# Kernel tuning notes

Measured on AMD Instinct MI355X. Metric: run time of the kernel, lower is better.

Reference implementation:

```python
import jax, jax.numpy as jnp
import numpy as np

SORB = 64      # spin orbitals (sequence length)
NELE = 32      # electrons
H = 512        # num_hiddens
B = 4096       # batch
ALPHA = NELE // 2                      # = beta = 16 (spin-up / spin-down electrons)
MIN_I = min(SORB - 2 * ALPHA, 2 * ALPHA)  # = 32; symmetry mask active for i >= MIN_I
EPS = 1e-12


def setup_inputs() -> dict:
    key = jax.random.key(0)
    ks = jax.random.split(key, 10)
    s_in = 1.0 / np.sqrt(2.0)
    s_h = 1.0 / np.sqrt(H)
    return {
        "x": jax.random.randint(ks[0], (B, SORB), 0, 2, dtype=jnp.int32),  # occupancies {0,1}
        "W_ih0": jax.random.normal(ks[1], (3 * H, 2), jnp.float32) * s_in,   # GRU layer0 input weights (r,z,n)
        "W_hh0": jax.random.normal(ks[2], (3 * H, H), jnp.float32) * s_h,
        "W_ih1": jax.random.normal(ks[3], (3 * H, H), jnp.float32) * s_h,    # GRU layer1
        "W_hh1": jax.random.normal(ks[4], (3 * H, H), jnp.float32) * s_h,
        "W_amp": jax.random.normal(ks[5], (2, H), jnp.float32) * s_h,
        "b_amp": jax.random.normal(ks[6], (2,), jnp.float32) * 0.01,
        "W_phase": jax.random.normal(ks[7], (2, H), jnp.float32) * s_h,
        "b_phase": jax.random.normal(ks[8], (2,), jnp.float32) * 0.01,
    }


def _gru_cell(x_in, h, Wih, Whh):
    # PyTorch GRU (bias=False), gate order r, z, n
    gi = x_in @ Wih.T          # (B, 3H)
    gh = h @ Whh.T             # (B, 3H)
    r = jax.nn.sigmoid(gi[:, :H] + gh[:, :H])
    z = jax.nn.sigmoid(gi[:, H:2 * H] + gh[:, H:2 * H])
    n = jnp.tanh(gi[:, 2 * H:] + r * gh[:, 2 * H:])
    return (1.0 - z) * n + z * h


def reference(x, W_ih0, W_hh0, W_ih1, W_hh1, W_amp, b_amp, W_phase, b_phase):
    dt = W_ih0.dtype
    bits = x.astype(jnp.int32)           # (B, SORB) occupancies
    nb = bits.shape[0]

    def step(carry, inp):
        h0, h1, x0, amp, phase, nup, ndn = carry
        i, b_i = inp                      # site index, occupancy bits (B,)
        h0n = _gru_cell(x0, h0, W_ih0, W_hh0)
        h1n = _gru_cell(h0n, h1, W_ih1, W_hh1)
        y = h1n                           # (B, H)
        # amplitude: sqrt(softmax(linear))
        y_amp = jnp.sqrt(jax.nn.softmax(y @ W_amp.T + b_amp, axis=1))   # (B, 2)
        # phase: pi * softsign(linear)
        ph = y @ W_phase.T + b_phase
        y_ph = jnp.pi * ph / (1.0 + jnp.abs(ph))
        # particle-number symmetry mask (alpha == beta spin sectors)
        is_even = (i % 2) == 0            # even sites: spin-up, odd: spin-down
        cnt = jnp.where(is_even, nup, ndn)
        lower = (ALPHA - SORB // 2 + i // 2).astype(dt)
        occ_ok = (cnt < ALPHA).astype(dt)
        unocc_ok = (cnt > lower).astype(dt)
        mask = jnp.stack([unocc_ok, occ_ok], axis=1)
        masked = y_amp * mask
        masked = masked / jnp.sqrt(jnp.sum(masked * masked, axis=1, keepdims=True) + EPS)
        y_amp = jnp.where(i >= MIN_I, masked, y_amp)
        # accumulate conditional amplitude / phase at the sampled occupancy
        sel_a = jnp.take_along_axis(y_amp, b_i[:, None], axis=1)[:, 0]
        sel_p = jnp.take_along_axis(y_ph, b_i[:, None], axis=1)[:, 0]
        amp = amp * sel_a
        phase = phase + sel_p
        bf = b_i.astype(dt)
        nup = nup + jnp.where(is_even, bf, 0.0)
        ndn = ndn + jnp.where(is_even, 0.0, bf)
        x0n = jax.nn.one_hot(b_i, 2, dtype=dt)  # next-step GRU input
        return (h0n, h1n, x0n, amp, phase, nup, ndn), None

    init = (
        jnp.zeros((nb, H), dt), jnp.zeros((nb, H), dt), jnp.zeros((nb, 2), dt),
        jnp.ones((nb,), dt), jnp.zeros((nb,), dt), jnp.zeros((nb,), dt), jnp.zeros((nb,), dt),
    )
    xs = (jnp.arange(SORB), bits.T)       # scan over sites
    (_, _, _, amp, phase, _, _), _ = jax.lax.scan(step, init, xs)
    # complex wavefunction psi = amp * exp(1j*phase); returned as real pair (amp, phase)
    return jnp.stack([amp, phase], axis=-1)
```

## Files before the change

kernel.cpp:

```cpp
#include <hip/hip_runtime.h>
#include <hip/hip_bf16.h>

#define SORB  64
#define HID   512
#define BATCH 4096
#define N3H   1536
#define KD    512
#define BK    64
#define PI_F  3.14159265358979f

typedef _Float16 half8 __attribute__((ext_vector_type(8)));
typedef float    floatx4 __attribute__((ext_vector_type(4)));

__device__ __forceinline__ void gload16(const void* g, void* l) {
    __builtin_amdgcn_global_load_lds(
        (const __attribute__((address_space(1))) void*)g,
        (__attribute__((address_space(3))) void*)l, 16, 0, 0);
}
#define SCHED_FENCE() __builtin_amdgcn_sched_barrier(0)

__device__ __forceinline__ float sigmoidf_(float x) { return 1.f / (1.f + __expf(-x)); }
__device__ __forceinline__ float tanhf_(float x) {
    x = fminf(fmaxf(x, -15.f), 15.f);
    const float e2 = __expf(2.f * x);
    return (e2 - 1.f) / (e2 + 1.f);
}

__global__ __launch_bounds__(256) void convw_kernel(
    const float* __restrict__ w0, const float* __restrict__ w1, const float* __restrict__ w2,
    _Float16* __restrict__ o0, _Float16* __restrict__ o1, _Float16* __restrict__ o2)
{
    const int i = blockIdx.x * 256 + threadIdx.x;
    if (i < N3H * KD) {
        o0[i] = (_Float16)w0[i];
        o1[i] = (_Float16)w1[i];
        o2[i] = (_Float16)w2[i];
    }
}

__global__ __launch_bounds__(256) void init_kernel(
    float* __restrict__ amp, float* __restrict__ phase,
    int* __restrict__ nup, int* __restrict__ ndn)
{
    const int i = blockIdx.x * 256 + threadIdx.x;
    if (i < BATCH) { amp[i] = 1.f; phase[i] = 0.f; nup[i] = 0; ndn[i] = 0; }
}

__global__ __launch_bounds__(256) void step1_kernel(
    const _Float16* __restrict__ h0h_c, const _Float16* __restrict__ wh0,
    const float* __restrict__ Wih0, const int* __restrict__ bits,
    _Float16* __restrict__ h0h_n, int step)
{
    const int j0 = blockIdx.x * 64;
    const int m0 = blockIdx.y * 64;

    __shared__ __align__(16) _Float16 Bs[2][192 * BK];

    const int tid  = threadIdx.x;
    const int lane = tid & 63;
    const int wid  = tid >> 6;
    const int wm   = wid >> 1, wj = wid & 1;
    const int ku   = lane >> 4;

    floatx4 acc[2][2][3];
    const floatx4 z4 = {0.f, 0.f, 0.f, 0.f};
#pragma unroll
    for (int a = 0; a < 2; ++a)
#pragma unroll
        for (int b = 0; b < 2; ++b)
#pragma unroll
            for (int g = 0; g < 3; ++g) acc[a][b][g] = z4;

    const _Float16* b_srcp[6];
#pragma unroll
    for (int k2 = 0; k2 < 6; ++k2) {
        const int p = tid + k2 * 256, row = p >> 3, c = (p & 7) ^ (row & 7);
        const int grow = (row >> 6) * HID + j0 + (row & 63);
        b_srcp[k2] = wh0 + (size_t)grow * KD + c * 8;
    }
    _Float16* b_dst0[6];
    _Float16* b_dst1[6];
#pragma unroll
    for (int k2 = 0; k2 < 6; ++k2) {
        b_dst0[k2] = Bs[0] + (size_t)(k2 * 256 + wid * 64) * 8;
        b_dst1[k2] = Bs[1] + (size_t)(k2 * 256 + wid * 64) * 8;
    }

    const _Float16* a_row[2];
#pragma unroll
    for (int mf = 0; mf < 2; ++mf)
        a_row[mf] = h0h_c + (size_t)(m0 + wm * 32 + mf * 16 + (lane & 15)) * KD + ku * 8;

    int boff[2][3][2];
#pragma unroll
    for (int jf = 0; jf < 2; ++jf)
#pragma unroll
        for (int g = 0; g < 3; ++g) {
            const int r = g * 64 + wj * 32 + jf * 16 + (lane & 15);
#pragma unroll
            for (int kk = 0; kk < 2; ++kk)
                boff[jf][g][kk] = r * BK + (((kk * 4 + ku) ^ (r & 7)) * 8);
        }

#pragma unroll
    for (int k2 = 0; k2 < 6; ++k2) gload16(b_srcp[k2], b_dst0[k2]);

#pragma unroll
    for (int kt = 0; kt < 8; ++kt) {
        half8 af[2][2];
#pragma unroll
        for (int mf = 0; mf < 2; ++mf)
#pragma unroll
            for (int kk = 0; kk < 2; ++kk)
                af[mf][kk] = *(const half8*)(a_row[mf] + kt * BK + kk * 32);
        if (kt < 7) {
#pragma unroll
            for (int k2 = 0; k2 < 6; ++k2)
                gload16(b_srcp[k2] + (kt + 1) * BK, ((kt & 1) ? b_dst0 : b_dst1)[k2]);
            asm volatile("s_waitcnt vmcnt(10)" ::: "memory");
        } else {
            asm volatile("s_waitcnt vmcnt(4)" ::: "memory");
        }
        SCHED_FENCE();
        __builtin_amdgcn_s_barrier();
        SCHED_FENCE();
        const _Float16* Bcur = Bs[kt & 1];
#pragma unroll
        for (int kk = 0; kk < 2; ++kk) {
            half8 bf[2][3];
#pragma unroll
            for (int jf = 0; jf < 2; ++jf)
#pragma unroll
                for (int g = 0; g < 3; ++g) bf[jf][g] = *(const half8*)(Bcur + boff[jf][g][kk]);
#pragma unroll
            for (int mf = 0; mf < 2; ++mf)
#pragma unroll
                for (int jf = 0; jf < 2; ++jf)
#pragma unroll
                    for (int g = 0; g < 3; ++g)
                        acc[mf][jf][g] = __builtin_amdgcn_mfma_f32_16x16x32_f16(
                            af[mf][kk], bf[jf][g], acc[mf][jf][g], 0, 0, 0);
        }
        SCHED_FENCE();
        asm volatile("s_waitcnt lgkmcnt(0)" ::: "memory");
        __builtin_amdgcn_s_barrier();
        SCHED_FENCE();
    }

#pragma unroll
    for (int mf = 0; mf < 2; ++mf)
#pragma unroll
        for (int jf = 0; jf < 2; ++jf) {
            const floatx4 gr = acc[mf][jf][0];
            const floatx4 gz = acc[mf][jf][1];
            const floatx4 gn = acc[mf][jf][2];
#pragma unroll
            for (int reg = 0; reg < 4; ++reg) {
                const int m = m0 + wm * 32 + mf * 16 + (lane >> 4) * 4 + reg;
                const int j = j0 + wj * 32 + jf * 16 + (lane & 15);
                float gir = 0.f, giz = 0.f, gin = 0.f;
                if (step > 0) {
                    const int tb = bits[m * SORB + step - 1];
                    gir = Wih0[j * 2 + tb];
                    giz = Wih0[(HID + j) * 2 + tb];
                    gin = Wih0[(2 * HID + j) * 2 + tb];
                }
                const float r  = sigmoidf_(gir + gr[reg]);
                const float zz = sigmoidf_(giz + gz[reg]);
                const float n  = tanhf_(gin + r * gn[reg]);
                const size_t idx = (size_t)m * HID + j;
                const float h  = (float)h0h_c[idx];
                h0h_n[idx] = (_Float16)((1.f - zz) * n + zz * h);
            }
        }
}

__global__ __launch_bounds__(256) void step2_kernel(
    const _Float16* __restrict__ h0h_n, const _Float16* __restrict__ h1h_c,
    const _Float16* __restrict__ wi1,   const _Float16* __restrict__ wh1,
    _Float16* __restrict__ h1h_n)
{
    const int j0 = blockIdx.x * 64;
    const int m0 = blockIdx.y * 64;

    __shared__ __align__(16) _Float16 Bs[2][192 * BK];

    const int tid  = threadIdx.x;
    const int lane = tid & 63;
    const int wid  = tid >> 6;
    const int wm   = wid >> 1, wj = wid & 1;
    const int ku   = lane >> 4;

    floatx4 acc[2][2][3];
    floatx4 accn[2][2];
    const floatx4 z4 = {0.f, 0.f, 0.f, 0.f};
#pragma unroll
    for (int a = 0; a < 2; ++a)
#pragma unroll
        for (int b = 0; b < 2; ++b) {
#pragma unroll
            for (int g = 0; g < 3; ++g) acc[a][b][g] = z4;
            accn[a][b] = z4;
        }

    const _Float16* Aops[2] = {h0h_n, h1h_c};
    const _Float16* Wops[2] = {wi1, wh1};
    const _Float16* b_srcH[2][6];
    const _Float16* a_rowH[2][2];
#pragma unroll
    for (int h = 0; h < 2; ++h) {
#pragma unroll
        for (int k2 = 0; k2 < 6; ++k2) {
            const int p = tid + k2 * 256, row = p >> 3, c = (p & 7) ^ (row & 7);
            const int grow = (row >> 6) * HID + j0 + (row & 63);
            b_srcH[h][k2] = Wops[h] + (size_t)grow * KD + c * 8;
        }
#pragma unroll
        for (int mf = 0; mf < 2; ++mf)
            a_rowH[h][mf] = Aops[h] + (size_t)(m0 + wm * 32 + mf * 16 + (lane & 15)) * KD + ku * 8;
    }
    _Float16* b_dst0[6];
    _Float16* b_dst1[6];
#pragma unroll
    for (int k2 = 0; k2 < 6; ++k2) {
        b_dst0[k2] = Bs[0] + (size_t)(k2 * 256 + wid * 64) * 8;
        b_dst1[k2] = Bs[1] + (size_t)(k2 * 256 + wid * 64) * 8;
    }

    int boff[2][3][2];
#pragma unroll
    for (int jf = 0; jf < 2; ++jf)
#pragma unroll
        for (int g = 0; g < 3; ++g) {
            const int r = g * 64 + wj * 32 + jf * 16 + (lane & 15);
#pragma unroll
            for (int kk = 0; kk < 2; ++kk)
                boff[jf][g][kk] = r * BK + (((kk * 4 + ku) ^ (r & 7)) * 8);
        }

#pragma unroll
    for (int k2 = 0; k2 < 6; ++k2) gload16(b_srcH[0][k2], b_dst0[k2]);

#pragma unroll
    for (int it = 0; it < 16; ++it) {
        const int half = it >> 3, kt = it & 7;
        half8 af[2][2];
#pragma unroll
        for (int mf = 0; mf < 2; ++mf)
#pragma unroll
            for (int kk = 0; kk < 2; ++kk)
                af[mf][kk] = *(const half8*)(a_rowH[half][mf] + kt * BK + kk * 32);
        if (it < 15) {
            const int nh = (it + 1) >> 3, nk = (it + 1) & 7;
#pragma unroll
            for (int k2 = 0; k2 < 6; ++k2)
                gload16(b_srcH[nh][k2] + nk * BK, ((it & 1) ? b_dst0 : b_dst1)[k2]);
            asm volatile("s_waitcnt vmcnt(10)" ::: "memory");
        } else {
            asm volatile("s_waitcnt vmcnt(4)" ::: "memory");
        }
        SCHED_FENCE();
        __builtin_amdgcn_s_barrier();
        SCHED_FENCE();
        const _Float16* Bcur = Bs[it & 1];
#pragma unroll
        for (int kk = 0; kk < 2; ++kk) {
            half8 bf[2][3];
#pragma unroll
            for (int jf = 0; jf < 2; ++jf)
#pragma unroll
                for (int g = 0; g < 3; ++g) bf[jf][g] = *(const half8*)(Bcur + boff[jf][g][kk]);
#pragma unroll
            for (int mf = 0; mf < 2; ++mf)
#pragma unroll
                for (int jf = 0; jf < 2; ++jf) {
                    acc[mf][jf][0] = __builtin_amdgcn_mfma_f32_16x16x32_f16(
                        af[mf][kk], bf[jf][0], acc[mf][jf][0], 0, 0, 0);
                    acc[mf][jf][1] = __builtin_amdgcn_mfma_f32_16x16x32_f16(
                        af[mf][kk], bf[jf][1], acc[mf][jf][1], 0, 0, 0);
                    if (half == 0)
                        acc[mf][jf][2] = __builtin_amdgcn_mfma_f32_16x16x32_f16(
                            af[mf][kk], bf[jf][2], acc[mf][jf][2], 0, 0, 0);
                    else
                        accn[mf][jf] = __builtin_amdgcn_mfma_f32_16x16x32_f16(
                            af[mf][kk], bf[jf][2], accn[mf][jf], 0, 0, 0);
                }
        }
        SCHED_FENCE();
        asm volatile("s_waitcnt lgkmcnt(0)" ::: "memory");
        __builtin_amdgcn_s_barrier();
        SCHED_FENCE();
    }

#pragma unroll
    for (int mf = 0; mf < 2; ++mf)
#pragma unroll
        for (int jf = 0; jf < 2; ++jf) {
            const floatx4 grz = acc[mf][jf][0];
            const floatx4 gzz = acc[mf][jf][1];
            const floatx4 gin = acc[mf][jf][2];
            const floatx4 ghn = accn[mf][jf];
#pragma unroll
            for (int reg = 0; reg < 4; ++reg) {
                const int m = m0 + wm * 32 + mf * 16 + (lane >> 4) * 4 + reg;
                const int j = j0 + wj * 32 + jf * 16 + (lane & 15);
                const float r  = sigmoidf_(grz[reg]);
                const float zz = sigmoidf_(gzz[reg]);
                const float n  = tanhf_(gin[reg] + r * ghn[reg]);
                const size_t idx = (size_t)m * HID + j;
                const float h  = (float)h1h_c[idx];
                h1h_n[idx] = (_Float16)((1.f - zz) * n + zz * h);
            }
        }
}

__global__ __launch_bounds__(256) void head_kernel(
    const _Float16* __restrict__ h1h_n,
    const float* __restrict__ Wamp, const float* __restrict__ bamp,
    const float* __restrict__ Wph,  const float* __restrict__ bph,
    const int* __restrict__ bits,
    float* __restrict__ amp, float* __restrict__ phase,
    int* __restrict__ nup, int* __restrict__ ndn,
    float* __restrict__ out, int step)
{
    const int lane = threadIdx.x & 63;
    const int m    = blockIdx.x * 4 + (threadIdx.x >> 6);
    const half8 hv = *(const half8*)(h1h_n + (size_t)m * HID + lane * 8);
    float d0 = 0.f, d1 = 0.f, d2 = 0.f, d3 = 0.f;
#pragma unroll
    for (int e = 0; e < 8; ++e) {
        const int j = lane * 8 + e;
        const float hn = (float)hv[e];
        d0 += hn * Wamp[j];       d1 += hn * Wamp[HID + j];
        d2 += hn * Wph[j];        d3 += hn * Wph[HID + j];
    }
#pragma unroll
    for (int off = 1; off < 64; off <<= 1) {
        d0 += __shfl_xor(d0, off); d1 += __shfl_xor(d1, off);
        d2 += __shfl_xor(d2, off); d3 += __shfl_xor(d3, off);
    }
    if (lane == 0) {
        const float a0 = d0 + bamp[0];
        const float a1 = d1 + bamp[1];
        const float mx = fmaxf(a0, a1);
        const float e0 = __expf(a0 - mx), e1 = __expf(a1 - mx);
        const float inv = 1.f / (e0 + e1);
        float ya0 = sqrtf(e0 * inv), ya1 = sqrtf(e1 * inv);
        const float p0 = d2 + bph[0];
        const float p1 = d3 + bph[1];
        const float yp0 = PI_F * p0 / (1.f + fabsf(p0));
        const float yp1 = PI_F * p1 / (1.f + fabsf(p1));
        const int even = ((step & 1) == 0);
        const int cnt = even ? nup[m] : ndn[m];
        if (step >= 32) {
            const int lower = (step >> 1) - 16;
            const float m0v = (cnt > lower) ? ya0 : 0.f;
            const float m1v = (cnt < 16) ? ya1 : 0.f;
            const float nrm = sqrtf(m0v * m0v + m1v * m1v + 1e-12f);
            ya0 = m0v / nrm; ya1 = m1v / nrm;
        }
        const int bi = bits[m * SORB + step];
        const float na = amp[m] * (bi ? ya1 : ya0);
        const float np = phase[m] + (bi ? yp1 : yp0);
        amp[m] = na; phase[m] = np;
        if (bi) { if (even) nup[m] = cnt + 1; else ndn[m] = cnt + 1; }
        if (step == SORB - 1) {
            out[m * 2 + 0] = na;
            out[m * 2 + 1] = np;
        }
    }
}

extern "C" void kernel_launch(void* const* d_in, const int* in_sizes, int n_in,
                              void* d_out, int out_size, void* d_ws, size_t ws_size,
                              hipStream_t stream) {
    const int*   bits = (const int*)d_in[0];
    const float* Wih0 = (const float*)d_in[1];
    const float* Whh0 = (const float*)d_in[2];
    const float* Wih1 = (const float*)d_in[3];
    const float* Whh1 = (const float*)d_in[4];
    const float* Wamp = (const float*)d_in[5];
    const float* bamp = (const float*)d_in[6];
    const float* Wph  = (const float*)d_in[7];
    const float* bph  = (const float*)d_in[8];
    float* out = (float*)d_out;

    char* ws = (char*)d_ws;
    size_t off = 0;
    auto alloc = [&](size_t bytes) {
        void* p = ws + off;
        off = (off + bytes + 255) & ~(size_t)255;
        return p;
    };
    _Float16* wh0 = (_Float16*)alloc((size_t)N3H * KD * 2);
    _Float16* wi1 = (_Float16*)alloc((size_t)N3H * KD * 2);
    _Float16* wh1 = (_Float16*)alloc((size_t)N3H * KD * 2);
    _Float16* h0hA = (_Float16*)alloc((size_t)BATCH * HID * 2);
    _Float16* h0hB = (_Float16*)alloc((size_t)BATCH * HID * 2);
    _Float16* h1hA = (_Float16*)alloc((size_t)BATCH * HID * 2);
    _Float16* h1hB = (_Float16*)alloc((size_t)BATCH * HID * 2);
    float*    amp   = (float*)alloc((size_t)BATCH * 4);
    float*    phase = (float*)alloc((size_t)BATCH * 4);
    int*      nup   = (int*)alloc((size_t)BATCH * 4);
    int*      ndn   = (int*)alloc((size_t)BATCH * 4);

    _Float16* h0h[2] = {h0hA, h0hB};
    _Float16* h1h[2] = {h1hA, h1hB};

    hipMemsetAsync(h0hA, 0, (size_t)BATCH * HID * 2, stream);
    hipMemsetAsync(h1hA, 0, (size_t)BATCH * HID * 2, stream);
    convw_kernel<<<(N3H * KD + 255) / 256, 256, 0, stream>>>(Whh0, Wih1, Whh1, wh0, wi1, wh1);
    init_kernel<<<BATCH / 256, 256, 0, stream>>>(amp, phase, nup, ndn);

    for (int s = 0; s < SORB; ++s) {
        const int cur = s & 1, nxt = cur ^ 1;
        step1_kernel<<<dim3(8, 64), 256, 0, stream>>>(
            h0h[cur], wh0, Wih0, bits, h0h[nxt], s);
        step2_kernel<<<dim3(8, 64), 256, 0, stream>>>(
            h0h[nxt], h1h[cur], wi1, wh1, h1h[nxt]);
        head_kernel<<<BATCH / 4, 256, 0, stream>>>(
            h1h[nxt], Wamp, bamp, Wph, bph, bits, amp, phase, nup, ndn, out, s);
    }
}
```

Measured before the change: 3.390 ms.

## Halve GRU GEMM row tile, stage A in LDS, drop double buffering

Both GRU step kernels now use a 32-row batch tile instead of 64, doubling the grid to 8x128 blocks, and each wave owns 16 output columns across all three gates instead of a 2x2 wave split. The A operand (hidden state) is now loaded into LDS with global_load_lds and a swizzle, rather than read directly from global memory into registers. The double-buffered B pipeline with manual vmcnt waits and sched barriers is replaced by a single buffer with __syncthreads before and after each k-tile. This raises occupancy and block count but halves weight reuse per block (more weight traffic) and removes load/compute overlap inside a block.

```diff
diff --git a/kernel.cpp b/kernel.cpp
--- a/kernel.cpp
+++ b/kernel.cpp
@@ -17,7 +17,6 @@
         (const __attribute__((address_space(1))) void*)g,
         (__attribute__((address_space(3))) void*)l, 16, 0, 0);
 }
-#define SCHED_FENCE() __builtin_amdgcn_sched_barrier(0)
 
 __device__ __forceinline__ float sigmoidf_(float x) { return 1.f / (1.f + __expf(-x)); }
 __device__ __forceinline__ float tanhf_(float x) {
@@ -52,25 +51,26 @@
     _Float16* __restrict__ h0h_n, int step)
 {
     const int j0 = blockIdx.x * 64;
-    const int m0 = blockIdx.y * 64;
-
-    __shared__ __align__(16) _Float16 Bs[2][192 * BK];
+    const int m0 = blockIdx.y * 32;
+
+    __shared__ __align__(16) _Float16 As[32 * BK];
+    __shared__ __align__(16) _Float16 Bs[192 * BK];
 
     const int tid  = threadIdx.x;
     const int lane = tid & 63;
     const int wid  = tid >> 6;
-    const int wm   = wid >> 1, wj = wid & 1;
     const int ku   = lane >> 4;
 
-    floatx4 acc[2][2][3];
+    floatx4 acc[2][3];
     const floatx4 z4 = {0.f, 0.f, 0.f, 0.f};
 #pragma unroll
     for (int a = 0; a < 2; ++a)
 #pragma unroll
-        for (int b = 0; b < 2; ++b)
-#pragma unroll
-            for (int g = 0; g < 3; ++g) acc[a][b][g] = z4;
-
+        for (int g = 0; g < 3; ++g) acc[a][g] = z4;
+
+    const int pa = tid, rowa = pa >> 3, ca = (pa & 7) ^ (rowa & 7);
+    const _Float16* a_src = h0h_c + (size_t)(m0 + rowa) * KD + ca * 8;
+    _Float16* a_dst = As + (size_t)(wid * 64) * 8;
     const _Float16* b_srcp[6];
 #pragma unroll
     for (int k2 = 0; k2 < 6; ++k2) {
@@ -78,101 +78,73 @@
         const int grow = (row >> 6) * HID + j0 + (row & 63);
         b_srcp[k2] = wh0 + (size_t)grow * KD + c * 8;
     }
-    _Float16* b_dst0[6];
-    _Float16* b_dst1[6];
-#pragma unroll
-    for (int k2 = 0; k2 < 6; ++k2) {
-        b_dst0[k2] = Bs[0] + (size_t)(k2 * 256 + wid * 64) * 8;
-        b_dst1[k2] = Bs[1] + (size_t)(k2 * 256 + wid * 64) * 8;
-    }
-
-    const _Float16* a_row[2];
-#pragma unroll
-    for (int mf = 0; mf < 2; ++mf)
-        a_row[mf] = h0h_c + (size_t)(m0 + wm * 32 + mf * 16 + (lane & 15)) * KD + ku * 8;
-
-    int boff[2][3][2];
-#pragma unroll
-    for (int jf = 0; jf < 2; ++jf)
-#pragma unroll
-        for (int g = 0; g < 3; ++g) {
-            const int r = g * 64 + wj * 32 + jf * 16 + (lane & 15);
-#pragma unroll
-            for (int kk = 0; kk < 2; ++kk)
-                boff[jf][g][kk] = r * BK + (((kk * 4 + ku) ^ (r & 7)) * 8);
-        }
-
-#pragma unroll
-    for (int k2 = 0; k2 < 6; ++k2) gload16(b_srcp[k2], b_dst0[k2]);
-
-#pragma unroll
+    _Float16* b_dst[6];
+#pragma unroll
+    for (int k2 = 0; k2 < 6; ++k2) b_dst[k2] = Bs + (size_t)(k2 * 256 + wid * 64) * 8;
+
+    int aoff[2][2], boff[3][2];
+#pragma unroll
+    for (int mf = 0; mf < 2; ++mf) {
+        const int r = mf * 16 + (lane & 15);
+#pragma unroll
+        for (int kk = 0; kk < 2; ++kk)
+            aoff[mf][kk] = r * BK + (((kk * 4 + ku) ^ (r & 7)) * 8);
+    }
+#pragma unroll
+    for (int g = 0; g < 3; ++g) {
+        const int r = g * 64 + wid * 16 + (lane & 15);
+#pragma unroll
+        for (int kk = 0; kk < 2; ++kk)
+            boff[g][kk] = r * BK + (((kk * 4 + ku) ^ (r & 7)) * 8);
+    }
+
     for (int kt = 0; kt < 8; ++kt) {
-        half8 af[2][2];
-#pragma unroll
-        for (int mf = 0; mf < 2; ++mf)
-#pragma unroll
-            for (int kk = 0; kk < 2; ++kk)
-                af[mf][kk] = *(const half8*)(a_row[mf] + kt * BK + kk * 32);
-        if (kt < 7) {
-#pragma unroll
-            for (int k2 = 0; k2 < 6; ++k2)
-                gload16(b_srcp[k2] + (kt + 1) * BK, ((kt & 1) ? b_dst0 : b_dst1)[k2]);
-            asm volatile("s_waitcnt vmcnt(10)" ::: "memory");
-        } else {
-            asm volatile("s_waitcnt vmcnt(4)" ::: "memory");
-        }
-        SCHED_FENCE();
-        __builtin_amdgcn_s_barrier();
-        SCHED_FENCE();
-        const _Float16* Bcur = Bs[kt & 1];
+        const int k0 = kt * BK;
+        gload16(a_src + k0, a_dst);
+#pragma unroll
+        for (int k2 = 0; k2 < 6; ++k2) gload16(b_srcp[k2] + k0, b_dst[k2]);
+        __syncthreads();
 #pragma unroll
         for (int kk = 0; kk < 2; ++kk) {
-            half8 bf[2][3];
-#pragma unroll
-            for (int jf = 0; jf < 2; ++jf)
-#pragma unroll
-                for (int g = 0; g < 3; ++g) bf[jf][g] = *(const half8*)(Bcur + boff[jf][g][kk]);
+            half8 af[2], bf[3];
+#pragma unroll
+            for (int mf = 0; mf < 2; ++mf) af[mf] = *(const half8*)(As + aoff[mf][kk]);
+#pragma unroll
+            for (int g = 0; g < 3; ++g) bf[g] = *(const half8*)(Bs + boff[g][kk]);
 #pragma unroll
             for (int mf = 0; mf < 2; ++mf)
 #pragma unroll
-                for (int jf = 0; jf < 2; ++jf)
-#pragma unroll
-                    for (int g = 0; g < 3; ++g)
-                        acc[mf][jf][g] = __builtin_amdgcn_mfma_f32_16x16x32_f16(
-                            af[mf][kk], bf[jf][g], acc[mf][jf][g], 0, 0, 0);
-        }
-        SCHED_FENCE();
-        asm volatile("s_waitcnt lgkmcnt(0)" ::: "memory");
-        __builtin_amdgcn_s_barrier();
-        SCHED_FENCE();
-    }
-
-#pragma unroll
-    for (int mf = 0; mf < 2; ++mf)
-#pragma unroll
-        for (int jf = 0; jf < 2; ++jf) {
-            const floatx4 gr = acc[mf][jf][0];
-            const floatx4 gz = acc[mf][jf][1];
-            const floatx4 gn = acc[mf][jf][2];
-#pragma unroll
-            for (int reg = 0; reg < 4; ++reg) {
-                const int m = m0 + wm * 32 + mf * 16 + (lane >> 4) * 4 + reg;
-                const int j = j0 + wj * 32 + jf * 16 + (lane & 15);
-                float gir = 0.f, giz = 0.f, gin = 0.f;
-                if (step > 0) {
-                    const int tb = bits[m * SORB + step - 1];
-                    gir = Wih0[j * 2 + tb];
-                    giz = Wih0[(HID + j) * 2 + tb];
-                    gin = Wih0[(2 * HID + j) * 2 + tb];
-                }
-                const float r  = sigmoidf_(gir + gr[reg]);
-                const float zz = sigmoidf_(giz + gz[reg]);
-                const float n  = tanhf_(gin + r * gn[reg]);
-                const size_t idx = (size_t)m * HID + j;
-                const float h  = (float)h0h_c[idx];
-                h0h_n[idx] = (_Float16)((1.f - zz) * n + zz * h);
+                for (int g = 0; g < 3; ++g)
+                    acc[mf][g] = __builtin_amdgcn_mfma_f32_16x16x32_f16(
+                        af[mf], bf[g], acc[mf][g], 0, 0, 0);
+        }
+        __syncthreads();
+    }
+
+#pragma unroll
+    for (int mf = 0; mf < 2; ++mf) {
+        const floatx4 gr = acc[mf][0];
+        const floatx4 gz = acc[mf][1];
+        const floatx4 gn = acc[mf][2];
+#pragma unroll
+        for (int reg = 0; reg < 4; ++reg) {
+            const int m = m0 + mf * 16 + (lane >> 4) * 4 + reg;
+            const int j = j0 + wid * 16 + (lane & 15);
+            float gir = 0.f, giz = 0.f, gin = 0.f;
+            if (step > 0) {
+                const int tb = bits[m * SORB + step - 1];
+                gir = Wih0[j * 2 + tb];
+                giz = Wih0[(HID + j) * 2 + tb];
+                gin = Wih0[(2 * HID + j) * 2 + tb];
             }
-        }
+            const float r  = sigmoidf_(gir + gr[reg]);
+            const float zz = sigmoidf_(giz + gz[reg]);
+            const float n  = tanhf_(gin + r * gn[reg]);
+            const size_t idx = (size_t)m * HID + j;
+            const float h  = (float)h0h_c[idx];
+            h0h_n[idx] = (_Float16)((1.f - zz) * n + zz * h);
+        }
+    }
 }
 
 __global__ __launch_bounds__(256) void step2_kernel(
@@ -181,137 +153,110 @@
     _Float16* __restrict__ h1h_n)
 {
     const int j0 = blockIdx.x * 64;
-    const int m0 = blockIdx.y * 64;
-
-    __shared__ __align__(16) _Float16 Bs[2][192 * BK];
+    const int m0 = blockIdx.y * 32;
+
+    __shared__ __align__(16) _Float16 As[32 * BK];
+    __shared__ __align__(16) _Float16 Bs[192 * BK];
 
     const int tid  = threadIdx.x;
     const int lane = tid & 63;
     const int wid  = tid >> 6;
-    const int wm   = wid >> 1, wj = wid & 1;
     const int ku   = lane >> 4;
 
-    floatx4 acc[2][2][3];
-    floatx4 accn[2][2];
+    floatx4 acc[2][3];
+    floatx4 accn[2];
     const floatx4 z4 = {0.f, 0.f, 0.f, 0.f};
 #pragma unroll
-    for (int a = 0; a < 2; ++a)
-#pragma unroll
-        for (int b = 0; b < 2; ++b) {
-#pragma unroll
-            for (int g = 0; g < 3; ++g) acc[a][b][g] = z4;
-            accn[a][b] = z4;
-        }
-
-    const _Float16* Aops[2] = {h0h_n, h1h_c};
-    const _Float16* Wops[2] = {wi1, wh1};
-    const _Float16* b_srcH[2][6];
-    const _Float16* a_rowH[2][2];
-#pragma unroll
-    for (int h = 0; h < 2; ++h) {
+    for (int a = 0; a < 2; ++a) {
+#pragma unroll
+        for (int g = 0; g < 3; ++g) acc[a][g] = z4;
+        accn[a] = z4;
+    }
+
+    _Float16* a_dst = As + (size_t)(wid * 64) * 8;
+    _Float16* b_dst[6];
+#pragma unroll
+    for (int k2 = 0; k2 < 6; ++k2) b_dst[k2] = Bs + (size_t)(k2 * 256 + wid * 64) * 8;
+
+    int aoff[2][2], boff[3][2];
+#pragma unroll
+    for (int mf = 0; mf < 2; ++mf) {
+        const int r = mf * 16 + (lane & 15);
+#pragma unroll
+        for (int kk = 0; kk < 2; ++kk)
+            aoff[mf][kk] = r * BK + (((kk * 4 + ku) ^ (r & 7)) * 8);
+    }
+#pragma unroll
+    for (int g = 0; g < 3; ++g) {
+        const int r = g * 64 + wid * 16 + (lane & 15);
+#pragma unroll
+        for (int kk = 0; kk < 2; ++kk)
+            boff[g][kk] = r * BK + (((kk * 4 + ku) ^ (r & 7)) * 8);
+    }
+
+#pragma unroll 1
+    for (int half = 0; half < 2; ++half) {
+        const _Float16* Aop = half ? h1h_c : h0h_n;
+        const _Float16* Wop = half ? wh1  : wi1;
+        const int pa = tid, rowa = pa >> 3, ca = (pa & 7) ^ (rowa & 7);
+        const _Float16* a_src = Aop + (size_t)(m0 + rowa) * KD + ca * 8;
+        const _Float16* b_srcp[6];
 #pragma unroll
         for (int k2 = 0; k2 < 6; ++k2) {
             const int p = tid + k2 * 256, row = p >> 3, c = (p & 7) ^ (row & 7);
             const int grow = (row >> 6) * HID + j0 + (row & 63);
-            b_srcH[h][k2] = Wops[h] + (size_t)grow * KD + c * 8;
-        }
-#pragma unroll
-        for (int mf = 0; mf < 2; ++mf)
-            a_rowH[h][mf] = Aops[h] + (size_t)(m0 + wm * 32 + mf * 16 + (lane & 15)) * KD + ku * 8;
-    }
-    _Float16* b_dst0[6];
-    _Float16* b_dst1[6];
-#pragma unroll
-    for (int k2 = 0; k2 < 6; ++k2) {
-        b_dst0[k2] = Bs[0] + (size_t)(k2 * 256 + wid * 64) * 8;
-        b_dst1[k2] = Bs[1] + (size_t)(k2 * 256 + wid * 64) * 8;
-    }
-
-    int boff[2][3][2];
-#pragma unroll
-    for (int jf = 0; jf < 2; ++jf)
-#pragma unroll
-        for (int g = 0; g < 3; ++g) {
-            const int r = g * 64 + wj * 32 + jf * 16 + (lane & 15);
-#pragma unroll
-            for (int kk = 0; kk < 2; ++kk)
-                boff[jf][g][kk] = r * BK + (((kk * 4 + ku) ^ (r & 7)) * 8);
-        }
-
-#pragma unroll
-    for (int k2 = 0; k2 < 6; ++k2) gload16(b_srcH[0][k2], b_dst0[k2]);
-
-#pragma unroll
-    for (int it = 0; it < 16; ++it) {
-        const int half = it >> 3, kt = it & 7;
-        half8 af[2][2];
-#pragma unroll
-        for (int mf = 0; mf < 2; ++mf)
-#pragma unroll
-            for (int kk = 0; kk < 2; ++kk)
-                af[mf][kk] = *(const half8*)(a_rowH[half][mf] + kt * BK + kk * 32);
-        if (it < 15) {
-            const int nh = (it + 1) >> 3, nk = (it + 1) & 7;
-#pragma unroll
-            for (int k2 = 0; k2 < 6; ++k2)
-                gload16(b_srcH[nh][k2] + nk * BK, ((it & 1) ? b_dst0 : b_dst1)[k2]);
-            asm volatile("s_waitcnt vmcnt(10)" ::: "memory");
-        } else {
-            asm volatile("s_waitcnt vmcnt(4)" ::: "memory");
-        }
-        SCHED_FENCE();
-        __builtin_amdgcn_s_barrier();
-        SCHED_FENCE();
-        const _Float16* Bcur = Bs[it & 1];
-#pragma unroll
-        for (int kk = 0; kk < 2; ++kk) {
-            half8 bf[2][3];
-#pragma unroll
-            for (int jf = 0; jf < 2; ++jf)
-#pragma unroll
-                for (int g = 0; g < 3; ++g) bf[jf][g] = *(const half8*)(Bcur + boff[jf][g][kk]);
-#pragma unroll
-            for (int mf = 0; mf < 2; ++mf)
-#pragma unroll
-                for (int jf = 0; jf < 2; ++jf) {
-                    acc[mf][jf][0] = __builtin_amdgcn_mfma_f32_16x16x32_f16(
-                        af[mf][kk], bf[jf][0], acc[mf][jf][0], 0, 0, 0);
-                    acc[mf][jf][1] = __builtin_amdgcn_mfma_f32_16x16x32_f16(
-                        af[mf][kk], bf[jf][1], acc[mf][jf][1], 0, 0, 0);
+            b_srcp[k2] = Wop + (size_t)grow * KD + c * 8;
+        }
+
+        for (int kt = 0; kt < 8; ++kt) {
+            const int k0 = kt * BK;
+            gload16(a_src + k0, a_dst);
+#pragma unroll
+            for (int k2 = 0; k2 < 6; ++k2) gload16(b_srcp[k2] + k0, b_dst[k2]);
+            __syncthreads();
+#pragma unroll
+            for (int kk = 0; kk < 2; ++kk) {
+                half8 af[2], bf[3];
+#pragma unroll
+                for (int mf = 0; mf < 2; ++mf) af[mf] = *(const half8*)(As + aoff[mf][kk]);
+#pragma unroll
+                for (int g = 0; g < 3; ++g) bf[g] = *(const half8*)(Bs + boff[g][kk]);
+#pragma unroll
+                for (int mf = 0; mf < 2; ++mf) {
+                    acc[mf][0] = __builtin_amdgcn_mfma_f32_16x16x32_f16(
+                        af[mf], bf[0], acc[mf][0], 0, 0, 0);
+                    acc[mf][1] = __builtin_amdgcn_mfma_f32_16x16x32_f16(
+                        af[mf], bf[1], acc[mf][1], 0, 0, 0);
                     if (half == 0)
-                        acc[mf][jf][2] = __builtin_amdgcn_mfma_f32_16x16x32_f16(
-                            af[mf][kk], bf[jf][2], acc[mf][jf][2], 0, 0, 0);
+                        acc[mf][2] = __builtin_amdgcn_mfma_f32_16x16x32_f16(
+                            af[mf], bf[2], acc[mf][2], 0, 0, 0);
                     else
-                        accn[mf][jf] = __builtin_amdgcn_mfma_f32_16x16x32_f16(
-                            af[mf][kk], bf[jf][2], accn[mf][jf], 0, 0, 0);
+                        accn[mf] = __builtin_amdgcn_mfma_f32_16x16x32_f16(
+                            af[mf], bf[2], accn[mf], 0, 0, 0);
                 }
-        }
-        SCHED_FENCE();
-        asm volatile("s_waitcnt lgkmcnt(0)" ::: "memory");
-        __builtin_amdgcn_s_barrier();
-        SCHED_FENCE();
-    }
-
-#pragma unroll
-    for (int mf = 0; mf < 2; ++mf)
-#pragma unroll
-        for (int jf = 0; jf < 2; ++jf) {
-            const floatx4 grz = acc[mf][jf][0];
-            const floatx4 gzz = acc[mf][jf][1];
-            const floatx4 gin = acc[mf][jf][2];
-            const floatx4 ghn = accn[mf][jf];
-#pragma unroll
-            for (int reg = 0; reg < 4; ++reg) {
-                const int m = m0 + wm * 32 + mf * 16 + (lane >> 4) * 4 + reg;
-                const int j = j0 + wj * 32 + jf * 16 + (lane & 15);
-                const float r  = sigmoidf_(grz[reg]);
-                const float zz = sigmoidf_(gzz[reg]);
-                const float n  = tanhf_(gin[reg] + r * ghn[reg]);
-                const size_t idx = (size_t)m * HID + j;
-                const float h  = (float)h1h_c[idx];
-                h1h_n[idx] = (_Float16)((1.f - zz) * n + zz * h);
             }
-        }
+            __syncthreads();
+        }
+    }
+
+#pragma unroll
+    for (int mf = 0; mf < 2; ++mf) {
+        const floatx4 grz = acc[mf][0];
+        const floatx4 gzz = acc[mf][1];
+        const floatx4 gin = acc[mf][2];
+        const floatx4 ghn = accn[mf];
+#pragma unroll
+        for (int reg = 0; reg < 4; ++reg) {
+            const int m = m0 + mf * 16 + (lane >> 4) * 4 + reg;
+            const int j = j0 + wid * 16 + (lane & 15);
+            const float r  = sigmoidf_(grz[reg]);
+            const float zz = sigmoidf_(gzz[reg]);
+            const float n  = tanhf_(gin[reg] + r * ghn[reg]);
+            const size_t idx = (size_t)m * HID + j;
+            const float h  = (float)h1h_c[idx];
+            h1h_n[idx] = (_Float16)((1.f - zz) * n + zz * h);
+        }
+    }
 }
 
 __global__ __launch_bounds__(256) void head_kernel(
@@ -414,9 +359,9 @@
 
     for (int s = 0; s < SORB; ++s) {
         const int cur = s & 1, nxt = cur ^ 1;
-        step1_kernel<<<dim3(8, 64), 256, 0, stream>>>(
+        step1_kernel<<<dim3(8, 128), 256, 0, stream>>>(
             h0h[cur], wh0, Wih0, bits, h0h[nxt], s);
-        step2_kernel<<<dim3(8, 64), 256, 0, stream>>>(
+        step2_kernel<<<dim3(8, 128), 256, 0, stream>>>(
             h0h[nxt], h1h[cur], wi1, wh1, h1h[nxt]);
         head_kernel<<<BATCH / 4, 256, 0, stream>>>(
             h1h[nxt], Wamp, bamp, Wph, bph, bits, amp, phase, nup, ndn, out, s);
```

Result: slower. 3.689 ms (+8.8%).
